# Optimization experiments

Hardware: AMD Instinct MI355X
Metric: run time of the kernel (lower is better)

## Reference

```python
import jax, jax.numpy as jnp
import numpy as np

V = 100000
E = 1250000
C_IN = 64
C_OUT = 64


def setup_inputs() -> dict:
    key = jax.random.key(0)
    ks = jax.random.split(key, 6)
    X = jax.random.normal(ks[0], (V, C_IN), dtype=jnp.float32)
    edge_src = jax.random.randint(ks[1], (E,), 0, V, dtype=jnp.int32)
    edge_dst = jax.random.randint(ks[2], (E,), 0, V, dtype=jnp.int32)
    edge_w = jax.random.uniform(ks[3], (E,), dtype=jnp.float32)
    # xavier_normal for (C_IN, C_OUT) weight
    std = float(np.sqrt(2.0 / (C_IN + C_OUT)))
    W = jax.random.normal(ks[4], (C_IN, C_OUT), dtype=jnp.float32) * std
    b = jax.random.normal(ks[5], (C_OUT,), dtype=jnp.float32) * 0.0  # bias init zeros
    return {"X": X, "edge_src": edge_src, "edge_dst": edge_dst,
            "edge_w": edge_w, "W": W, "b": b}


def reference(X, edge_src, edge_dst, edge_w, W, b):
    # f = A @ X  (sparse COO spmm): f[dst] += w * X[src]
    msgs = edge_w[:, None] * X[edge_src]                 # [E, C_IN]
    f = jax.ops.segment_sum(msgs, edge_dst, num_segments=X.shape[0])  # [V, C_IN]
    # out = f @ W + b
    return f @ W + b
```

## Files before the change

kernel.cpp:

```cpp
#include <hip/hip_runtime.h>
#include <hip/hip_fp16.h>


constexpr int V = 100000;
constexpr int E = 1250000;
constexpr int C = 64;

constexpr int NBKT = 1024;
constexpr int VB   = 98;
constexpr int BCAP = 1536;
constexpr int FL   = 8;
constexpr int OVF_CAP = 16384;

constexpr size_t Y_OFF    = 0;
constexpr size_t BIN_OFF  = 12800000;
constexpr size_t GCNT_OFF = 25382912;
constexpr size_t OC_OFF   = 25387008;
constexpr size_t OVF_OFF  = 25387024;
constexpr size_t WS_NEW   = 25649168;

using bf16x8 = __attribute__((ext_vector_type(8))) short;
using f32x4  = __attribute__((ext_vector_type(4))) float;

__device__ __forceinline__ short f2bf(float x) {
    unsigned u = __float_as_uint(x);
    unsigned r = u + 0x7fffu + ((u >> 16) & 1u);
    return (short)(r >> 16);
}
__device__ __forceinline__ float bf2f(short h) {
    return __uint_as_float(((unsigned)(unsigned short)h) << 16);
}

constexpr int ZB  = 1;
constexpr int NBM = 1563;

__global__ __launch_bounds__(256) void zero_xw_kernel(const float* __restrict__ X,
                                                      const float* __restrict__ W,
                                                      __half* __restrict__ Y,
                                                      int* __restrict__ gcnt,
                                                      int* __restrict__ oc) {
    if (blockIdx.x < ZB) {
        int i = threadIdx.x;
        #pragma unroll
        for (int j = 0; j < NBKT / 256; ++j) gcnt[i + j * 256] = 0;
        if (i == 0) *oc = 0;
        return;
    }
    __shared__ short Whi[64 * 72];
    __shared__ short Wlo[64 * 72];
    for (int idx = threadIdx.x; idx < 4096; idx += 256) {
        int k = idx >> 6, c = idx & 63;
        float w  = W[idx];
        short hi = f2bf(w);
        short lo = f2bf(w - bf2f(hi));
        Whi[c * 72 + k] = hi;
        Wlo[c * 72 + k] = lo;
    }
    __syncthreads();

    const int wave = threadIdx.x >> 6;
    const int lane = threadIdx.x & 63;
    const int m = lane & 15;
    const int q = lane >> 4;

    bf16x8 bhi[4][2], blo[4][2];
    #pragma unroll
    for (int t = 0; t < 4; ++t)
        #pragma unroll
        for (int h = 0; h < 2; ++h) {
            int o = (t * 16 + m) * 72 + h * 32 + q * 8;
            bhi[t][h] = *(const bf16x8*)&Whi[o];
            blo[t][h] = *(const bf16x8*)&Wlo[o];
        }

    const int chunk = (blockIdx.x - ZB) * 4 + wave;
    if (chunk >= V / 16) return;
    {
        const float* xp = X + (chunk * 16 + m) * 64 + q * 8;
        bf16x8 ahi[2], alo[2];
        #pragma unroll
        for (int h = 0; h < 2; ++h) {
            float4 f0 = *(const float4*)(xp + h * 32);
            float4 f1 = *(const float4*)(xp + h * 32 + 4);
            float f[8] = {f0.x, f0.y, f0.z, f0.w, f1.x, f1.y, f1.z, f1.w};
            #pragma unroll
            for (int j = 0; j < 8; ++j) {
                short hi = f2bf(f[j]);
                ahi[h][j] = hi;
                alo[h][j] = f2bf(f[j] - bf2f(hi));
            }
        }
        #pragma unroll
        for (int t = 0; t < 4; ++t) {
            f32x4 acc = {0.f, 0.f, 0.f, 0.f};
            #pragma unroll
            for (int h = 0; h < 2; ++h) {
                acc = __builtin_amdgcn_mfma_f32_16x16x32_bf16(ahi[h], bhi[t][h], acc, 0, 0, 0);
                acc = __builtin_amdgcn_mfma_f32_16x16x32_bf16(alo[h], bhi[t][h], acc, 0, 0, 0);
                acc = __builtin_amdgcn_mfma_f32_16x16x32_bf16(ahi[h], blo[t][h], acc, 0, 0, 0);
            }
            #pragma unroll
            for (int i = 0; i < 4; ++i) {
                int row = chunk * 16 + q * 4 + i;
                Y[row * 64 + t * 16 + m] = __float2half(acc[i]);
            }
        }
    }
}

constexpr int BIN_BLOCKS = 512;
constexpr int BIN_T      = 1024;

__global__ __launch_bounds__(BIN_T) void bin_kernel(const int*   __restrict__ esrc,
                                                    const int*   __restrict__ edst,
                                                    const float* __restrict__ ew,
                                                    int*  __restrict__ gcnt,
                                                    int2* __restrict__ binned,
                                                    int*  __restrict__ oc,
                                                    int4* __restrict__ ovf) {
    __shared__ int2 stage[NBKT][FL];
    __shared__ int  lcnt[NBKT];
    for (int i = threadIdx.x; i < NBKT; i += BIN_T) lcnt[i] = 0;
    __syncthreads();

    const int iters = (E + BIN_BLOCKS * BIN_T - 1) / (BIN_BLOCKS * BIN_T);
    for (int it = 0; it < iters; ++it) {
        int e = (it * BIN_BLOCKS + blockIdx.x) * BIN_T + threadIdx.x;
        if (e < E) {
            int d = edst[e];
            int s = esrc[e];
            float w = ew[e];
            int bkt = d / VB;
            int ld  = d - bkt * VB;
            int2 rec = make_int2((ld << 17) | s, __float_as_int(w));
            int pos = atomicAdd(&lcnt[bkt], 1);
            if (pos < FL) {
                stage[bkt][pos] = rec;
            } else {
                int g = atomicAdd(&gcnt[bkt], 1);
                if (g < BCAP) binned[bkt * BCAP + g] = rec;
                else { int p = atomicAdd(oc, 1);
                       if (p < OVF_CAP) ovf[p] = make_int4(s, d, __float_as_int(w), 0); }
            }
        }
    }
    __syncthreads();
    for (int b = threadIdx.x; b < NBKT; b += BIN_T) {
        int n = lcnt[b]; n = n < FL ? n : FL;
        if (n > 0) {
            int g = atomicAdd(&gcnt[b], n);
            for (int i = 0; i < n; ++i) {
                int gi = g + i;
                int2 r = stage[b][i];
                if (gi < BCAP) binned[b * BCAP + gi] = r;
                else { int s = r.x & 0x1FFFF; int ld = r.x >> 17;
                       int p = atomicAdd(oc, 1);
                       if (p < OVF_CAP) ovf[p] = make_int4(s, b * VB + ld, r.y, 0); }
            }
        }
    }
}

__global__ __launch_bounds__(512) void bucket_gather_kernel(const int*  __restrict__ gcnt,
                                                            const int2* __restrict__ binned,
                                                            const int*  __restrict__ oc,
                                                            const int4* __restrict__ ovf,
                                                            const __half* __restrict__ Y,
                                                            const float* __restrict__ bias,
                                                            float* __restrict__ out) {
    __shared__ int2 raw[BCAP];
    __shared__ int2 sorted[BCAP];
    __shared__ int  cnt[VB];
    __shared__ int  pre[VB];
    __shared__ int  cur[VB];
    __shared__ int  buf[128];

    const int tid = threadIdx.x;
    const int b   = blockIdx.x;
    int n = gcnt[b]; n = n < BCAP ? n : BCAP;

    for (int i = tid; i < VB; i += 512) cnt[i] = 0;
    __syncthreads();

    const int2* src = binned + b * BCAP;
    for (int i = tid; i < n; i += 512) {
        int2 r = src[i];
        raw[i] = r;
        atomicAdd(&cnt[r.x >> 17], 1);
    }
    __syncthreads();

    int x = 0;
    if (tid < 128) { x = (tid < VB) ? cnt[tid] : 0; buf[tid] = x; }
    __syncthreads();
    #pragma unroll
    for (int ofs = 1; ofs < 128; ofs <<= 1) {
        int t = 0;
        if (tid < 128 && tid >= ofs) t = buf[tid - ofs];
        __syncthreads();
        if (tid < 128) buf[tid] += t;
        __syncthreads();
    }
    if (tid < VB) { int ex = buf[tid] - x; pre[tid] = ex; cur[tid] = ex; }
    __syncthreads();

    for (int i = tid; i < n; i += 512) {
        int2 r = raw[i];
        int ld = r.x >> 17;
        int p = atomicAdd(&cur[ld], 1);
        sorted[p] = r;
    }
    __syncthreads();

    const int lane = tid & 63;
    const int wv   = tid >> 6;
    float bias_l = bias[lane];
    int ovn = *oc; ovn = ovn < OVF_CAP ? ovn : OVF_CAP;

    for (int ld = wv; ld < VB; ld += 8) {
        int v = b * VB + ld;
        if (v >= V) break;
        int beg = pre[ld];
        int end = beg + cnt[ld];
        float acc = 0.f;
        int i = beg;
        for (; i + 8 <= end; i += 8) {
            int2 r0 = sorted[i],     r1 = sorted[i + 1];
            int2 r2 = sorted[i + 2], r3 = sorted[i + 3];
            int2 r4 = sorted[i + 4], r5 = sorted[i + 5];
            int2 r6 = sorted[i + 6], r7 = sorted[i + 7];
            float y0 = __half2float(Y[(r0.x & 0x1FFFF) * C + lane]);
            float y1 = __half2float(Y[(r1.x & 0x1FFFF) * C + lane]);
            float y2 = __half2float(Y[(r2.x & 0x1FFFF) * C + lane]);
            float y3 = __half2float(Y[(r3.x & 0x1FFFF) * C + lane]);
            float y4 = __half2float(Y[(r4.x & 0x1FFFF) * C + lane]);
            float y5 = __half2float(Y[(r5.x & 0x1FFFF) * C + lane]);
            float y6 = __half2float(Y[(r6.x & 0x1FFFF) * C + lane]);
            float y7 = __half2float(Y[(r7.x & 0x1FFFF) * C + lane]);
            acc += __int_as_float(r0.y) * y0;
            acc += __int_as_float(r1.y) * y1;
            acc += __int_as_float(r2.y) * y2;
            acc += __int_as_float(r3.y) * y3;
            acc += __int_as_float(r4.y) * y4;
            acc += __int_as_float(r5.y) * y5;
            acc += __int_as_float(r6.y) * y6;
            acc += __int_as_float(r7.y) * y7;
        }
        for (; i + 4 <= end; i += 4) {
            int2 r0 = sorted[i], r1 = sorted[i + 1], r2 = sorted[i + 2], r3 = sorted[i + 3];
            float y0 = __half2float(Y[(r0.x & 0x1FFFF) * C + lane]);
            float y1 = __half2float(Y[(r1.x & 0x1FFFF) * C + lane]);
            float y2 = __half2float(Y[(r2.x & 0x1FFFF) * C + lane]);
            float y3 = __half2float(Y[(r3.x & 0x1FFFF) * C + lane]);
            acc += __int_as_float(r0.y) * y0;
            acc += __int_as_float(r1.y) * y1;
            acc += __int_as_float(r2.y) * y2;
            acc += __int_as_float(r3.y) * y3;
        }
        for (; i < end; ++i) {
            int2 rr = sorted[i];
            acc += __int_as_float(rr.y) * __half2float(Y[(rr.x & 0x1FFFF) * C + lane]);
        }
        for (int k = 0; k < ovn; ++k) {
            int4 rr = ovf[k];
            if (rr.y == v)
                acc += __int_as_float(rr.z) * __half2float(Y[rr.x * C + lane]);
        }
        out[v * C + lane] = acc + bias_l;
    }
}

__global__ __launch_bounds__(256) void xw_kernel(const float* __restrict__ X,
                                                 const float* __restrict__ W,
                                                 float* __restrict__ Y) {
    __shared__ float Ws[64][64];
    const float4* W4 = (const float4*)W;
    float4* Ws4 = (float4*)&Ws[0][0];
    #pragma unroll
    for (int i = 0; i < 4; ++i)
        Ws4[threadIdx.x + 256 * i] = W4[threadIdx.x + 256 * i];
    __syncthreads();
    const int wave = threadIdx.x >> 6;
    const int lane = threadIdx.x & 63;
    for (int row = blockIdx.x * 4 + wave; row < V; row += gridDim.x * 4) {
        float xv = X[row * C + lane];
        float acc = 0.f;
        #pragma unroll
        for (int k = 0; k < C; ++k)
            acc += __shfl(xv, k, 64) * Ws[k][lane];
        Y[row * C + lane] = acc;
    }
}

__global__ __launch_bounds__(256) void init_out_kernel(const float* __restrict__ b,
                                                       float4* __restrict__ out4) {
    int tid = blockIdx.x * 256 + threadIdx.x;
    const int n4 = V * (C / 4);
    if (tid < n4) {
        const float4* b4 = (const float4*)b;
        out4[tid] = b4[tid & 15];
    }
}

__global__ __launch_bounds__(256) void scatter_kernel(const int*   __restrict__ esrc,
                                                      const int*   __restrict__ edst,
                                                      const float* __restrict__ ew,
                                                      const float* __restrict__ Y,
                                                      float*       __restrict__ out) {
    unsigned tid = blockIdx.x * 256u + threadIdx.x;
    unsigned e = tid >> 4;
    if (e >= (unsigned)E) return;
    int g = (tid & 15) * 4;
    int   s  = esrc[e];
    int   d  = edst[e];
    float we = ew[e];
    float4 y = *(const float4*)(Y + s * C + g);
    float* o = out + (size_t)d * C + g;
    atomicAdd(o + 0, we * y.x);
    atomicAdd(o + 1, we * y.y);
    atomicAdd(o + 2, we * y.z);
    atomicAdd(o + 3, we * y.w);
}

extern "C" void kernel_launch(void* const* d_in, const int* in_sizes, int n_in,
                              void* d_out, int out_size, void* d_ws, size_t ws_size,
                              hipStream_t stream) {
    const float* X    = (const float*)d_in[0];
    const int*   esrc = (const int*)  d_in[1];
    const int*   edst = (const int*)  d_in[2];
    const float* ew   = (const float*)d_in[3];
    const float* W    = (const float*)d_in[4];
    const float* b    = (const float*)d_in[5];
    float* out = (float*)d_out;

    char* ws = (char*)d_ws;

    if (ws_size >= WS_NEW) {
        __half* Y     = (__half*)(ws + Y_OFF);
        int2*  binned = (int2*)(ws + BIN_OFF);
        int*   gcnt   = (int*) (ws + GCNT_OFF);
        int*   oc     = (int*) (ws + OC_OFF);
        int4*  ovf    = (int4*)(ws + OVF_OFF);

        zero_xw_kernel<<<ZB + NBM, 256, 0, stream>>>(X, W, Y, gcnt, oc);
        bin_kernel<<<BIN_BLOCKS, BIN_T, 0, stream>>>(esrc, edst, ew, gcnt, binned, oc, ovf);
        bucket_gather_kernel<<<NBKT, 512, 0, stream>>>(gcnt, binned, oc, ovf, Y, b, out);
    } else {
        float* Y = (float*)(ws + Y_OFF);
        xw_kernel<<<1024, 256, 0, stream>>>(X, W, Y);
        init_out_kernel<<<(V * (C / 4) + 255) / 256, 256, 0, stream>>>(b, (float4*)out);
        scatter_kernel<<<(E * 16 + 255) / 256, 256, 0, stream>>>(esrc, edst, ew, Y, out);
    }
}
```

Measured before the change: 143.8 us.

## Merge XW and binning into one launch with per-block fixed bucket segments

Fuses the X@W MFMA kernel and the edge binning kernel into one launch, with blocks split by role. Binning no longer uses global atomics. Each bin block writes a fixed 8-entry segment per bucket, a byte count, and a per-block overflow stash. The gather kernel then compacts these with a 512-way prefix scan and pulls in matching stash records, which replaces the linear scan over a global overflow list. This removes the zeroing pass, the global atomic contention and one launch, at the cost of a larger workspace, more scattered segment reads and extra scan syncs in the gather kernel.

```diff
diff --git a/kernel.cpp b/kernel.cpp
--- a/kernel.cpp
+++ b/kernel.cpp
@@ -8,16 +8,18 @@
 
 constexpr int NBKT = 1024;
 constexpr int VB   = 98;
-constexpr int BCAP = 1536;
-constexpr int FL   = 8;
-constexpr int OVF_CAP = 16384;
+constexpr int SEG  = 8;
+constexpr int BIN_BLOCKS = 512;
+constexpr int EPB  = (E + BIN_BLOCKS - 1) / BIN_BLOCKS;
+constexpr int STASH_CAP = 256;
+constexpr int BCAPL = 1792;
 
 constexpr size_t Y_OFF    = 0;
 constexpr size_t BIN_OFF  = 12800000;
-constexpr size_t GCNT_OFF = 25382912;
-constexpr size_t OC_OFF   = 25387008;
-constexpr size_t OVF_OFF  = 25387024;
-constexpr size_t WS_NEW   = 25649168;
+constexpr size_t CNT8_OFF = 46354432;
+constexpr size_t OVFC_OFF = 46878720;
+constexpr size_t OVFR_OFF = 46880768;
+constexpr size_t WS_NEW   = 48977920;
 
 using bf16x8 = __attribute__((ext_vector_type(8))) short;
 using f32x4  = __attribute__((ext_vector_type(4))) float;
@@ -31,51 +33,52 @@
     return __uint_as_float(((unsigned)(unsigned short)h) << 16);
 }
 
-constexpr int ZB  = 1;
-constexpr int NBM = 1563;
-
-__global__ __launch_bounds__(256) void zero_xw_kernel(const float* __restrict__ X,
+constexpr int XW_BLOCKS = 391;
+
+__global__ __launch_bounds__(1024) void xw_bin_kernel(const float* __restrict__ X,
                                                       const float* __restrict__ W,
+                                                      const int*   __restrict__ esrc,
+                                                      const int*   __restrict__ edst,
+                                                      const float* __restrict__ ew,
                                                       __half* __restrict__ Y,
-                                                      int* __restrict__ gcnt,
-                                                      int* __restrict__ oc) {
-    if (blockIdx.x < ZB) {
-        int i = threadIdx.x;
+                                                      int2*  __restrict__ binned,
+                                                      unsigned char* __restrict__ cnt8,
+                                                      int*   __restrict__ ovfcnt,
+                                                      int4*  __restrict__ ovfrec) {
+    __shared__ alignas(16) char smem[73744];
+    const int tid = threadIdx.x;
+
+    if (blockIdx.x < XW_BLOCKS) {
+        short* Whi = (short*)smem;
+        short* Wlo = (short*)(smem + 18432);
+        for (int idx = tid; idx < 4096; idx += 1024) {
+            int k = idx >> 6, c = idx & 63;
+            float w  = W[idx];
+            short hi = f2bf(w);
+            short lo = f2bf(w - bf2f(hi));
+            Whi[c * 72 + k] = hi;
+            Wlo[c * 72 + k] = lo;
+        }
+        __syncthreads();
+
+        const int wave = tid >> 6;
+        const int lane = tid & 63;
+        const int m = lane & 15;
+        const int q = lane >> 4;
+
+        const int chunk = blockIdx.x * 16 + wave;
+        if (chunk >= V / 16) return;
+
+        bf16x8 bhi[4][2], blo[4][2];
         #pragma unroll
-        for (int j = 0; j < NBKT / 256; ++j) gcnt[i + j * 256] = 0;
-        if (i == 0) *oc = 0;
-        return;
-    }
-    __shared__ short Whi[64 * 72];
-    __shared__ short Wlo[64 * 72];
-    for (int idx = threadIdx.x; idx < 4096; idx += 256) {
-        int k = idx >> 6, c = idx & 63;
-        float w  = W[idx];
-        short hi = f2bf(w);
-        short lo = f2bf(w - bf2f(hi));
-        Whi[c * 72 + k] = hi;
-        Wlo[c * 72 + k] = lo;
-    }
-    __syncthreads();
-
-    const int wave = threadIdx.x >> 6;
-    const int lane = threadIdx.x & 63;
-    const int m = lane & 15;
-    const int q = lane >> 4;
-
-    bf16x8 bhi[4][2], blo[4][2];
-    #pragma unroll
-    for (int t = 0; t < 4; ++t)
-        #pragma unroll
-        for (int h = 0; h < 2; ++h) {
-            int o = (t * 16 + m) * 72 + h * 32 + q * 8;
-            bhi[t][h] = *(const bf16x8*)&Whi[o];
-            blo[t][h] = *(const bf16x8*)&Wlo[o];
-        }
-
-    const int chunk = (blockIdx.x - ZB) * 4 + wave;
-    if (chunk >= V / 16) return;
-    {
+        for (int t = 0; t < 4; ++t)
+            #pragma unroll
+            for (int h = 0; h < 2; ++h) {
+                int o = (t * 16 + m) * 72 + h * 32 + q * 8;
+                bhi[t][h] = *(const bf16x8*)&Whi[o];
+                blo[t][h] = *(const bf16x8*)&Wlo[o];
+            }
+
         const float* xp = X + (chunk * 16 + m) * 64 + q * 8;
         bf16x8 ahi[2], alo[2];
         #pragma unroll
@@ -105,109 +108,128 @@
                 Y[row * 64 + t * 16 + m] = __float2half(acc[i]);
             }
         }
-    }
-}
-
-constexpr int BIN_BLOCKS = 512;
-constexpr int BIN_T      = 1024;
-
-__global__ __launch_bounds__(BIN_T) void bin_kernel(const int*   __restrict__ esrc,
-                                                    const int*   __restrict__ edst,
-                                                    const float* __restrict__ ew,
-                                                    int*  __restrict__ gcnt,
-                                                    int2* __restrict__ binned,
-                                                    int*  __restrict__ oc,
-                                                    int4* __restrict__ ovf) {
-    __shared__ int2 stage[NBKT][FL];
-    __shared__ int  lcnt[NBKT];
-    for (int i = threadIdx.x; i < NBKT; i += BIN_T) lcnt[i] = 0;
-    __syncthreads();
-
-    const int iters = (E + BIN_BLOCKS * BIN_T - 1) / (BIN_BLOCKS * BIN_T);
-    for (int it = 0; it < iters; ++it) {
-        int e = (it * BIN_BLOCKS + blockIdx.x) * BIN_T + threadIdx.x;
-        if (e < E) {
-            int d = edst[e];
-            int s = esrc[e];
-            float w = ew[e];
-            int bkt = d / VB;
-            int ld  = d - bkt * VB;
-            int2 rec = make_int2((ld << 17) | s, __float_as_int(w));
-            int pos = atomicAdd(&lcnt[bkt], 1);
-            if (pos < FL) {
-                stage[bkt][pos] = rec;
-            } else {
-                int g = atomicAdd(&gcnt[bkt], 1);
-                if (g < BCAP) binned[bkt * BCAP + g] = rec;
-                else { int p = atomicAdd(oc, 1);
-                       if (p < OVF_CAP) ovf[p] = make_int4(s, d, __float_as_int(w), 0); }
-            }
-        }
-    }
-    __syncthreads();
-    for (int b = threadIdx.x; b < NBKT; b += BIN_T) {
-        int n = lcnt[b]; n = n < FL ? n : FL;
-        if (n > 0) {
-            int g = atomicAdd(&gcnt[b], n);
-            for (int i = 0; i < n; ++i) {
-                int gi = g + i;
-                int2 r = stage[b][i];
-                if (gi < BCAP) binned[b * BCAP + gi] = r;
-                else { int s = r.x & 0x1FFFF; int ld = r.x >> 17;
-                       int p = atomicAdd(oc, 1);
-                       if (p < OVF_CAP) ovf[p] = make_int4(s, b * VB + ld, r.y, 0); }
-            }
-        }
-    }
-}
-
-__global__ __launch_bounds__(512) void bucket_gather_kernel(const int*  __restrict__ gcnt,
-                                                            const int2* __restrict__ binned,
-                                                            const int*  __restrict__ oc,
-                                                            const int4* __restrict__ ovf,
+        return;
+    }
+
+    int2* stage  = (int2*)smem;
+    int*  lcnt   = (int*)(smem + 65536);
+    int4* stash  = (int4*)(smem + 69632);
+    int*  stashN = (int*)(smem + 73728);
+
+    const int blk = blockIdx.x - XW_BLOCKS;
+    for (int i = tid; i < NBKT; i += 1024) lcnt[i] = 0;
+    if (tid == 0) *stashN = 0;
+    __syncthreads();
+
+    const int beg = blk * EPB;
+    const int end = (beg + EPB < E) ? beg + EPB : E;
+    for (int e = beg + tid; e < end; e += 1024) {
+        int d = edst[e];
+        int s = esrc[e];
+        float w = ew[e];
+        int bkt = d / VB;
+        int ld  = d - bkt * VB;
+        int pos = atomicAdd(&lcnt[bkt], 1);
+        if (pos < SEG) {
+            stage[bkt * SEG + pos] = make_int2((ld << 17) | s, __float_as_int(w));
+        } else {
+            int p = atomicAdd(stashN, 1);
+            if (p < STASH_CAP) stash[p] = make_int4(s, d, __float_as_int(w), 0);
+        }
+    }
+    __syncthreads();
+
+    {
+        const int b = tid;
+        int4* dst = (int4*)(binned + ((size_t)b * BIN_BLOCKS + blk) * SEG);
+        const int4* s4 = (const int4*)(stage + b * SEG);
+        dst[0] = s4[0]; dst[1] = s4[1]; dst[2] = s4[2]; dst[3] = s4[3];
+        int n = lcnt[b];
+        cnt8[blk * NBKT + b] = (unsigned char)(n < SEG ? n : SEG);
+    }
+    int sn = *stashN; sn = sn < STASH_CAP ? sn : STASH_CAP;
+    if (tid == 0) ovfcnt[blk] = sn;
+    for (int k = tid; k < sn; k += 1024) ovfrec[blk * STASH_CAP + k] = stash[k];
+}
+
+__global__ __launch_bounds__(512) void bucket_gather_kernel(const int2* __restrict__ binned,
+                                                            const unsigned char* __restrict__ cnt8,
+                                                            const int*  __restrict__ ovfcnt,
+                                                            const int4* __restrict__ ovfrec,
                                                             const __half* __restrict__ Y,
                                                             const float* __restrict__ bias,
                                                             float* __restrict__ out) {
-    __shared__ int2 raw[BCAP];
-    __shared__ int2 sorted[BCAP];
+    __shared__ int2 raw[BCAPL];
+    __shared__ int2 sorted[BCAPL];
     __shared__ int  cnt[VB];
     __shared__ int  pre[VB];
     __shared__ int  cur[VB];
-    __shared__ int  buf[128];
+    __shared__ int  sbuf[512];
+    __shared__ int  spillN;
 
     const int tid = threadIdx.x;
     const int b   = blockIdx.x;
-    int n = gcnt[b]; n = n < BCAP ? n : BCAP;
+    const int lo  = b * VB;
 
     for (int i = tid; i < VB; i += 512) cnt[i] = 0;
-    __syncthreads();
-
-    const int2* src = binned + b * BCAP;
-    for (int i = tid; i < n; i += 512) {
-        int2 r = src[i];
-        raw[i] = r;
-        atomicAdd(&cnt[r.x >> 17], 1);
-    }
+
+    int c = (int)cnt8[tid * NBKT + b];
+    sbuf[tid] = c;
+    __syncthreads();
+    #pragma unroll
+    for (int ofs = 1; ofs < 512; ofs <<= 1) {
+        int t = (tid >= ofs) ? sbuf[tid - ofs] : 0;
+        __syncthreads();
+        sbuf[tid] += t;
+        __syncthreads();
+    }
+    const int myoff = sbuf[tid] - c;
+    const int n = sbuf[511];
+
+    if (c > 0) {
+        const int2* segp = binned + ((size_t)b * BIN_BLOCKS + tid) * SEG;
+        for (int j = 0; j < c; ++j) {
+            int p = myoff + j;
+            if (p < BCAPL) raw[p] = segp[j];
+        }
+    }
+    if (tid == 0) spillN = (n < BCAPL) ? n : BCAPL;
+    __syncthreads();
+
+    {
+        int sc = ovfcnt[tid];
+        for (int k = 0; k < sc; ++k) {
+            int4 r = ovfrec[tid * STASH_CAP + k];
+            int ld = r.y - lo;
+            if (ld >= 0 && ld < VB) {
+                int p = atomicAdd(&spillN, 1);
+                if (p < BCAPL) raw[p] = make_int2((ld << 17) | r.x, r.z);
+            }
+        }
+    }
+    __syncthreads();
+    int ntot = spillN; ntot = ntot < BCAPL ? ntot : BCAPL;
+
+    for (int i = tid; i < ntot; i += 512) atomicAdd(&cnt[raw[i].x >> 17], 1);
     __syncthreads();
 
     int x = 0;
-    if (tid < 128) { x = (tid < VB) ? cnt[tid] : 0; buf[tid] = x; }
+    if (tid < 128) { x = (tid < VB) ? cnt[tid] : 0; sbuf[tid] = x; }
     __syncthreads();
     #pragma unroll
     for (int ofs = 1; ofs < 128; ofs <<= 1) {
         int t = 0;
-        if (tid < 128 && tid >= ofs) t = buf[tid - ofs];
-        __syncthreads();
-        if (tid < 128) buf[tid] += t;
-        __syncthreads();
-    }
-    if (tid < VB) { int ex = buf[tid] - x; pre[tid] = ex; cur[tid] = ex; }
-    __syncthreads();
-
-    for (int i = tid; i < n; i += 512) {
+        if (tid < 128 && tid >= ofs) t = sbuf[tid - ofs];
+        __syncthreads();
+        if (tid < 128) sbuf[tid] += t;
+        __syncthreads();
+    }
+    if (tid < VB) { int ex = sbuf[tid] - x; pre[tid] = ex; cur[tid] = ex; }
+    __syncthreads();
+
+    for (int i = tid; i < ntot; i += 512) {
         int2 r = raw[i];
-        int ld = r.x >> 17;
-        int p = atomicAdd(&cur[ld], 1);
+        int p = atomicAdd(&cur[r.x >> 17], 1);
         sorted[p] = r;
     }
     __syncthreads();
@@ -215,10 +237,9 @@
     const int lane = tid & 63;
     const int wv   = tid >> 6;
     float bias_l = bias[lane];
-    int ovn = *oc; ovn = ovn < OVF_CAP ? ovn : OVF_CAP;
 
     for (int ld = wv; ld < VB; ld += 8) {
-        int v = b * VB + ld;
+        int v = lo + ld;
         if (v >= V) break;
         int beg = pre[ld];
         int end = beg + cnt[ld];
@@ -261,11 +282,6 @@
             int2 rr = sorted[i];
             acc += __int_as_float(rr.y) * __half2float(Y[(rr.x & 0x1FFFF) * C + lane]);
         }
-        for (int k = 0; k < ovn; ++k) {
-            int4 rr = ovf[k];
-            if (rr.y == v)
-                acc += __int_as_float(rr.z) * __half2float(Y[rr.x * C + lane]);
-        }
         out[v * C + lane] = acc + bias_l;
     }
 }
@@ -336,15 +352,16 @@
     char* ws = (char*)d_ws;
 
     if (ws_size >= WS_NEW) {
-        __half* Y     = (__half*)(ws + Y_OFF);
-        int2*  binned = (int2*)(ws + BIN_OFF);
-        int*   gcnt   = (int*) (ws + GCNT_OFF);
-        int*   oc     = (int*) (ws + OC_OFF);
-        int4*  ovf    = (int4*)(ws + OVF_OFF);
-
-        zero_xw_kernel<<<ZB + NBM, 256, 0, stream>>>(X, W, Y, gcnt, oc);
-        bin_kernel<<<BIN_BLOCKS, BIN_T, 0, stream>>>(esrc, edst, ew, gcnt, binned, oc, ovf);
-        bucket_gather_kernel<<<NBKT, 512, 0, stream>>>(gcnt, binned, oc, ovf, Y, b, out);
+        __half* Y            = (__half*)(ws + Y_OFF);
+        int2*  binned        = (int2*)(ws + BIN_OFF);
+        unsigned char* cnt8  = (unsigned char*)(ws + CNT8_OFF);
+        int*   ovfcnt        = (int*) (ws + OVFC_OFF);
+        int4*  ovfrec        = (int4*)(ws + OVFR_OFF);
+
+        xw_bin_kernel<<<XW_BLOCKS + BIN_BLOCKS, 1024, 0, stream>>>(
+            X, W, esrc, edst, ew, Y, binned, cnt8, ovfcnt, ovfrec);
+        bucket_gather_kernel<<<NBKT, 512, 0, stream>>>(
+            binned, cnt8, ovfcnt, ovfrec, Y, b, out);
     } else {
         float* Y = (float*)(ws + Y_OFF);
         xw_kernel<<<1024, 256, 0, stream>>>(X, W, Y);
```

New measurement: 148.5 us. 3.2% more time.

## Replace per-bucket shared-memory sort with LDS float atomic accumulation tile

Applied to the files above, without the earlier changes.

The gather kernel no longer counting-sorts each bucket's edges by local destination. Edges are now processed in their raw order, and each product is accumulated with shared-memory float atomicAdd into a per-bucket VB×64 tile, which is then written out with bias. This removes the count, prefix-scan and scatter passes and their barriers, and spreads edges evenly across waves instead of per-destination loops. The cost is LDS atomic contention and a larger shared-memory footprint (about 25KB tile), which may lower occupancy; the float summation order also becomes nondeterministic.

```diff
diff --git a/kernel.cpp b/kernel.cpp
--- a/kernel.cpp
+++ b/kernel.cpp
@@ -168,67 +168,30 @@
                                                             const __half* __restrict__ Y,
                                                             const float* __restrict__ bias,
                                                             float* __restrict__ out) {
-    __shared__ int2 raw[BCAP];
-    __shared__ int2 sorted[BCAP];
-    __shared__ int  cnt[VB];
-    __shared__ int  pre[VB];
-    __shared__ int  cur[VB];
-    __shared__ int  buf[128];
-
-    const int tid = threadIdx.x;
-    const int b   = blockIdx.x;
-    int n = gcnt[b]; n = n < BCAP ? n : BCAP;
-
-    for (int i = tid; i < VB; i += 512) cnt[i] = 0;
-    __syncthreads();
-
-    const int2* src = binned + b * BCAP;
-    for (int i = tid; i < n; i += 512) {
-        int2 r = src[i];
-        raw[i] = r;
-        atomicAdd(&cnt[r.x >> 17], 1);
-    }
-    __syncthreads();
-
-    int x = 0;
-    if (tid < 128) { x = (tid < VB) ? cnt[tid] : 0; buf[tid] = x; }
-    __syncthreads();
-    #pragma unroll
-    for (int ofs = 1; ofs < 128; ofs <<= 1) {
-        int t = 0;
-        if (tid < 128 && tid >= ofs) t = buf[tid - ofs];
-        __syncthreads();
-        if (tid < 128) buf[tid] += t;
-        __syncthreads();
-    }
-    if (tid < VB) { int ex = buf[tid] - x; pre[tid] = ex; cur[tid] = ex; }
-    __syncthreads();
-
-    for (int i = tid; i < n; i += 512) {
-        int2 r = raw[i];
-        int ld = r.x >> 17;
-        int p = atomicAdd(&cur[ld], 1);
-        sorted[p] = r;
-    }
-    __syncthreads();
-
+    __shared__ int2  raw[BCAP];
+    __shared__ float tile[VB * C];
+
+    const int tid  = threadIdx.x;
+    const int b    = blockIdx.x;
     const int lane = tid & 63;
     const int wv   = tid >> 6;
-    float bias_l = bias[lane];
-    int ovn = *oc; ovn = ovn < OVF_CAP ? ovn : OVF_CAP;
-
-    for (int ld = wv; ld < VB; ld += 8) {
-        int v = b * VB + ld;
-        if (v >= V) break;
-        int beg = pre[ld];
-        int end = beg + cnt[ld];
-        float acc = 0.f;
-        int i = beg;
-        for (; i + 8 <= end; i += 8) {
-            int2 r0 = sorted[i],     r1 = sorted[i + 1];
-            int2 r2 = sorted[i + 2], r3 = sorted[i + 3];
-            int2 r4 = sorted[i + 4], r5 = sorted[i + 5];
-            int2 r6 = sorted[i + 6], r7 = sorted[i + 7];
+    const int lo   = b * VB;
+
+    int n = gcnt[b]; n = n < BCAP ? n : BCAP;
+
+    float4 z = {0.f, 0.f, 0.f, 0.f};
+    for (int i = tid; i < VB * C / 4; i += 512) ((float4*)tile)[i] = z;
+    const int2* src = binned + b * BCAP;
+    for (int i = tid; i < n; i += 512) raw[i] = src[i];
+    __syncthreads();
+
+    for (int base = wv * 8; base < n; base += 64) {
+        int m = n - base; m = m < 8 ? m : 8;
+        if (m == 8) {
+            int2 r0 = raw[base + 0], r1 = raw[base + 1];
+            int2 r2 = raw[base + 2], r3 = raw[base + 3];
+            int2 r4 = raw[base + 4], r5 = raw[base + 5];
+            int2 r6 = raw[base + 6], r7 = raw[base + 7];
             float y0 = __half2float(Y[(r0.x & 0x1FFFF) * C + lane]);
             float y1 = __half2float(Y[(r1.x & 0x1FFFF) * C + lane]);
             float y2 = __half2float(Y[(r2.x & 0x1FFFF) * C + lane]);
@@ -237,36 +200,38 @@
             float y5 = __half2float(Y[(r5.x & 0x1FFFF) * C + lane]);
             float y6 = __half2float(Y[(r6.x & 0x1FFFF) * C + lane]);
             float y7 = __half2float(Y[(r7.x & 0x1FFFF) * C + lane]);
-            acc += __int_as_float(r0.y) * y0;
-            acc += __int_as_float(r1.y) * y1;
-            acc += __int_as_float(r2.y) * y2;
-            acc += __int_as_float(r3.y) * y3;
-            acc += __int_as_float(r4.y) * y4;
-            acc += __int_as_float(r5.y) * y5;
-            acc += __int_as_float(r6.y) * y6;
-            acc += __int_as_float(r7.y) * y7;
-        }
-        for (; i + 4 <= end; i += 4) {
-            int2 r0 = sorted[i], r1 = sorted[i + 1], r2 = sorted[i + 2], r3 = sorted[i + 3];
-            float y0 = __half2float(Y[(r0.x & 0x1FFFF) * C + lane]);
-            float y1 = __half2float(Y[(r1.x & 0x1FFFF) * C + lane]);
-            float y2 = __half2float(Y[(r2.x & 0x1FFFF) * C + lane]);
-            float y3 = __half2float(Y[(r3.x & 0x1FFFF) * C + lane]);
-            acc += __int_as_float(r0.y) * y0;
-            acc += __int_as_float(r1.y) * y1;
-            acc += __int_as_float(r2.y) * y2;
-            acc += __int_as_float(r3.y) * y3;
-        }
-        for (; i < end; ++i) {
-            int2 rr = sorted[i];
-            acc += __int_as_float(rr.y) * __half2float(Y[(rr.x & 0x1FFFF) * C + lane]);
-        }
-        for (int k = 0; k < ovn; ++k) {
-            int4 rr = ovf[k];
-            if (rr.y == v)
-                acc += __int_as_float(rr.z) * __half2float(Y[rr.x * C + lane]);
-        }
-        out[v * C + lane] = acc + bias_l;
+            atomicAdd(&tile[(r0.x >> 17) * C + lane], __int_as_float(r0.y) * y0);
+            atomicAdd(&tile[(r1.x >> 17) * C + lane], __int_as_float(r1.y) * y1);
+            atomicAdd(&tile[(r2.x >> 17) * C + lane], __int_as_float(r2.y) * y2);
+            atomicAdd(&tile[(r3.x >> 17) * C + lane], __int_as_float(r3.y) * y3);
+            atomicAdd(&tile[(r4.x >> 17) * C + lane], __int_as_float(r4.y) * y4);
+            atomicAdd(&tile[(r5.x >> 17) * C + lane], __int_as_float(r5.y) * y5);
+            atomicAdd(&tile[(r6.x >> 17) * C + lane], __int_as_float(r6.y) * y6);
+            atomicAdd(&tile[(r7.x >> 17) * C + lane], __int_as_float(r7.y) * y7);
+        } else {
+            for (int j = 0; j < m; ++j) {
+                int2 r = raw[base + j];
+                float yv = __half2float(Y[(r.x & 0x1FFFF) * C + lane]);
+                atomicAdd(&tile[(r.x >> 17) * C + lane], __int_as_float(r.y) * yv);
+            }
+        }
+    }
+
+    int ovn = *oc; ovn = ovn < OVF_CAP ? ovn : OVF_CAP;
+    for (int k = wv; k < ovn; k += 8) {
+        int4 r = ovf[k];
+        int ld = r.y - lo;
+        if (ld >= 0 && ld < VB) {
+            float yv = __half2float(Y[r.x * C + lane]);
+            atomicAdd(&tile[ld * C + lane], __int_as_float(r.z) * yv);
+        }
+    }
+    __syncthreads();
+
+    float bias_l = bias[lane];
+    for (int i = tid; i < VB * C; i += 512) {
+        int v = lo + (i >> 6);
+        if (v < V) out[v * C + lane] = tile[i] + bias_l;
     }
 }
 
```

Measured after the change: 533.8 us. +271.1%, slower.
